# Optimization experiments

Measured on AMD Instinct MI355X. Metric: run time of the kernel, lower is better.

Reference implementation:

```python
import jax, jax.numpy as jnp
import numpy as np

# config (matches SS2Dv2 defaults: d_model=96, d_state=16, ssm_ratio=2.0, dt_rank=auto=6, k_group=4)
DM, DI, N, K, R = 96, 192, 16, 4, 6
BSZ, H_, W_ = 1, 56, 56


def setup_inputs() -> dict:
    key = jax.random.key(0)
    ks = jax.random.split(key, 8)
    return {
        "x": jax.random.normal(ks[0], (BSZ, H_, W_, DM), jnp.float32),
        "in_proj_w": jax.random.normal(ks[1], (2 * DI, DM), jnp.float32) / np.sqrt(DM).astype(np.float32),
        "conv_w": jax.random.normal(ks[2], (DI, 1, 3, 3), jnp.float32) * 0.1,
        "conv_b": jnp.zeros((DI,), jnp.float32),
        "x_proj_w": jax.random.normal(ks[3], (K, R + 2 * N, DI), jnp.float32) / np.sqrt(DI).astype(np.float32),
        "dt_projs_w": 0.1 * jax.random.uniform(ks[4], (K, DI, R), jnp.float32),
        "dt_projs_bias": 0.1 * jax.random.uniform(ks[5], (K, DI), jnp.float32),
        "A_logs": jnp.zeros((K * DI, N), jnp.float32),
        "Ds": jnp.ones((K * DI,), jnp.float32),
        "ln_w": jnp.ones((DI,), jnp.float32),
        "ln_b": jnp.zeros((DI,), jnp.float32),
        "out_proj_w": jax.random.normal(ks[6], (DM, DI), jnp.float32) / np.sqrt(DI).astype(np.float32),
    }


def _cross_scan(x):
    # x: (B, D, H, W) -> (B, 4, D, L); dirs: row-major, col-major, and their flips
    B, D, H, W = x.shape
    L = H * W
    x0 = x.reshape(B, D, L)
    x1 = jnp.swapaxes(x, 2, 3).reshape(B, D, L)
    return jnp.stack([x0, x1, x0[..., ::-1], x1[..., ::-1]], axis=1)


def _cross_merge(ys, H, W):
    # ys: (B, K, D, L) -> (B, D, L); invert each scan direction and sum
    B, Kk, D, L = ys.shape
    y0 = ys[:, 0]
    y2 = ys[:, 2][..., ::-1]
    y1 = jnp.swapaxes(ys[:, 1].reshape(B, D, W, H), 2, 3).reshape(B, D, L)
    y3 = jnp.swapaxes(ys[:, 3][..., ::-1].reshape(B, D, W, H), 2, 3).reshape(B, D, L)
    return y0 + y1 + y2 + y3


def _forward(x, in_proj_w, conv_w, conv_b, x_proj_w, dt_projs_w, dt_projs_bias,
             A_logs, Ds, ln_w, ln_b, out_proj_w):
    B, H, W, _ = x.shape
    L = H * W
    # in_proj + gate split (channel_first=False -> last dim)
    xz = jnp.einsum('bhwc,oc->bhwo', x, in_proj_w)
    xc, z = jnp.split(xz, 2, axis=-1)
    z = jax.nn.silu(z)
    # depthwise conv (NCHW)
    xc = jnp.transpose(xc, (0, 3, 1, 2))
    xc = jax.lax.conv_general_dilated(
        xc, conv_w, (1, 1), 'SAME', feature_group_count=DI,
        dimension_numbers=('NCHW', 'OIHW', 'NCHW')) + conv_b[None, :, None, None]
    xc = jax.nn.silu(xc)
    # 4-directional cross scan
    xs = _cross_scan(xc)  # (B,K,D,L)
    # grouped x_proj: per direction D -> R+2N
    x_dbl = jnp.einsum('bkdl,krd->bkrl', xs, x_proj_w)
    dts, Bs, Cs = jnp.split(x_dbl, [R, R + N], axis=2)  # (B,K,R,L),(B,K,N,L),(B,K,N,L)
    # grouped dt proj: per direction R -> D
    dts = jnp.einsum('bkrl,kdr->bkdl', dts, dt_projs_w)
    A = -jnp.exp(A_logs.astype(jnp.float32)).reshape(K, DI, N)
    delta = jax.nn.softplus(dts + dt_projs_bias[None, :, :, None])  # (B,K,D,L)
    # S6 selective scan: h_t = exp(delta*A)*h_{t-1} + delta*B*u, y_t = C.h_t + D*u
    dA = jnp.exp(jnp.einsum('bkdl,kdn->bkdln', delta, A))
    dBu = jnp.einsum('bkdl,bknl,bkdl->bkdln', delta, Bs, xs)

    def comb(e1, e2):
        a1, b1 = e1
        a2, b2 = e2
        return a2 * a1, a2 * b1 + b2

    _, h = jax.lax.associative_scan(comb, (dA, dBu), axis=3)  # (B,K,D,L,N)
    y = jnp.einsum('bkdln,bknl->bkdl', h, Cs) + Ds.reshape(K, DI)[None, :, :, None] * xs
    y = _cross_merge(y, H, W).reshape(B, DI, H, W)
    # out_norm: LayerNorm over channels (channel_first=False path)
    y = jnp.transpose(y, (0, 2, 3, 1))  # (B,H,W,D)
    mu = y.mean(-1, keepdims=True)
    var = ((y - mu) ** 2).mean(-1, keepdims=True)
    y = (y - mu) / jnp.sqrt(var + 1e-5) * ln_w + ln_b
    y = y * z
    return jnp.einsum('bhwd,od->bhwo', y, out_proj_w)


def reference(x, in_proj_w, conv_w, conv_b, x_proj_w, dt_projs_w, dt_projs_bias,
              A_logs, Ds, ln_w, ln_b, out_proj_w):
    return _forward(x, in_proj_w, conv_w, conv_b, x_proj_w, dt_projs_w, dt_projs_bias,
                    A_logs, Ds, ln_w, ln_b, out_proj_w)
```

## Files before the change

### kernel.cpp

```cpp
#include <hip/hip_runtime.h>
#include <hip/hip_bf16.h>
#include <math.h>

#define DM 96
#define DI 192
#define NS 16
#define KK 4
#define RR 6
#define HH 56
#define WW 56
#define LL (HH*WW)
#define RN (RR + 2*NS)
#define NCH 64
#define CLL (LL/NCH)

__device__ __forceinline__ float silu_f(float x) { return x / (1.f + __expf(-x)); }
__device__ __forceinline__ float softplus_f(float x) {
    return (x > 20.f) ? x : log1pf(__expf(x));
}

__global__ __launch_bounds__(256) void k_inproj(
        const float* __restrict__ x, const float* __restrict__ w,
        float* __restrict__ xc_t, float* __restrict__ z_nat) {
    __shared__ float xt[32 * 100];
    __shared__ float wt[32 * 100];
    const int l0 = blockIdx.x * 32;
    const int o0 = blockIdx.y * 32;
    const int tid = threadIdx.x;
    for (int i = tid; i < 32 * 24; i += 256) {
        int r = i / 24, q = i % 24;
        *(float4*)&xt[r * 100 + 4 * q] = *(const float4*)&x[(size_t)(l0 + r) * DM + 4 * q];
        *(float4*)&wt[r * 100 + 4 * q] = *(const float4*)&w[(size_t)(o0 + r) * DM + 4 * q];
    }
    __syncthreads();
    const int tx = tid & 15, ty = tid >> 4;
    float acc[2][2] = {};
    for (int c = 0; c < 96; c += 4) {
        float4 av[2], bv[2];
#pragma unroll
        for (int i = 0; i < 2; ++i) av[i] = *(const float4*)&xt[(ty + 16 * i) * 100 + c];
#pragma unroll
        for (int j = 0; j < 2; ++j) bv[j] = *(const float4*)&wt[(tx + 16 * j) * 100 + c];
#pragma unroll
        for (int i = 0; i < 2; ++i)
#pragma unroll
            for (int j = 0; j < 2; ++j) {
                acc[i][j] = fmaf(av[i].x, bv[j].x, acc[i][j]);
                acc[i][j] = fmaf(av[i].y, bv[j].y, acc[i][j]);
                acc[i][j] = fmaf(av[i].z, bv[j].z, acc[i][j]);
                acc[i][j] = fmaf(av[i].w, bv[j].w, acc[i][j]);
            }
    }
    __syncthreads();
    float* ot = xt;
#pragma unroll
    for (int j = 0; j < 2; ++j)
#pragma unroll
        for (int i = 0; i < 2; ++i)
            ot[(tx + 16 * j) * 65 + (ty + 16 * i)] = acc[i][j];
    __syncthreads();
    if (o0 < DI) {
        for (int i = tid; i < 32 * 32; i += 256) {
            int ol = i >> 5, ll = i & 31;
            xc_t[(size_t)(o0 + ol) * LL + l0 + ll] = ot[ol * 65 + ll];
        }
    } else {
        for (int i = tid; i < 32 * 32; i += 256) {
            int ll = i >> 5, ol = i & 31;
            z_nat[(size_t)(l0 + ll) * DI + (o0 - DI) + ol] = silu_f(ot[ol * 65 + ll]);
        }
    }
}

__global__ __launch_bounds__(256) void k_convT(
        const float* __restrict__ xc_t, const float* __restrict__ cw,
        const float* __restrict__ cb, float* __restrict__ xconv, float* __restrict__ xs1) {
    __shared__ float in_s[16 * 56];
    __shared__ float out_s[14 * 57];
    const int d = blockIdx.x;
    const int h0 = blockIdx.y * 14;
    const int tid = threadIdx.x;
    const float* in = xc_t + (size_t)d * LL;
    for (int i = tid; i < 16 * 14; i += 256) {
        int row = i / 14, q = i % 14;
        int r = row - 1 + h0;
        float4 v = make_float4(0.f, 0.f, 0.f, 0.f);
        if (r >= 0 && r < HH) v = *(const float4*)&in[r * WW + 4 * q];
        *(float4*)&in_s[row * 56 + 4 * q] = v;
    }
    __syncthreads();
    const float b0 = cb[d];
    float w9[9];
#pragma unroll
    for (int i = 0; i < 9; ++i) w9[i] = cw[d * 9 + i];
    for (int i = tid; i < 14 * 56; i += 256) {
        int hh = i / 56, w = i % 56;
        float acc = b0;
#pragma unroll
        for (int di = 0; di < 3; ++di)
#pragma unroll
            for (int dj = 0; dj < 3; ++dj) {
                int w2 = w + dj - 1;
                if (w2 < 0 || w2 >= WW) continue;
                acc = fmaf(in_s[(hh + di) * 56 + w2], w9[di * 3 + dj], acc);
            }
        acc = silu_f(acc);
        xconv[(size_t)d * LL + (h0 + hh) * WW + w] = acc;
        out_s[hh * 57 + w] = acc;
    }
    __syncthreads();
    for (int i = tid; i < 14 * 56; i += 256) {
        int w = i / 14, hh = i % 14;
        xs1[(size_t)d * LL + w * HH + h0 + hh] = out_s[hh * 57 + w];
    }
}

__global__ __launch_bounds__(256) void k_xdblD(
        const float* __restrict__ xconv, const float* __restrict__ xs1,
        const float* __restrict__ pw, const float* __restrict__ dtw,
        const float* __restrict__ dtb,
        float* __restrict__ Bn, float* __restrict__ Cn, float* __restrict__ delta) {
    __shared__ float xt[DI * 16];
    __shared__ float wk_s[32 * DI];
    __shared__ float dtS[RR * 17];
    const int k = blockIdx.y;
    const int l0 = blockIdx.x * 16;
    const int tid = threadIdx.x;
    const float* in = (k & 1) ? xs1 : xconv;
    const float* wk = pw + (size_t)k * RN * DI;
    for (int i = tid; i < DI * 4; i += 256) {
        int d = i >> 2, q = i & 3;
        *(float4*)&xt[(d << 4) + 4 * q] = *(const float4*)&in[(size_t)d * LL + l0 + 4 * q];
    }
    {
        const float4* src = (const float4*)(wk + RR * DI);
        float4* dst = (float4*)wk_s;
        for (int i = tid; i < (32 * DI) / 4; i += 256) dst[i] = src[i];
    }
    __syncthreads();
    if (tid < RR * 16) {
        int r = tid >> 4, lx = tid & 15;
        const float* wr = wk + r * DI;
        float acc = 0.f;
#pragma unroll 8
        for (int d = 0; d < DI; ++d) acc = fmaf(xt[(d << 4) + lx], wr[d], acc);
        dtS[r * 17 + lx] = acc;
    }
    {
        const int sx = tid & 15, cg = tid >> 4;
        float acc2[2] = {};
        for (int d = 0; d < DI; d += 4) {
            float x0 = xt[(d + 0) * 16 + sx];
            float x1 = xt[(d + 1) * 16 + sx];
            float x2 = xt[(d + 2) * 16 + sx];
            float x3 = xt[(d + 3) * 16 + sx];
#pragma unroll
            for (int j = 0; j < 2; ++j) {
                float4 wv = *(const float4*)&wk_s[(cg + 16 * j) * DI + d];
                acc2[j] = fmaf(x0, wv.x, acc2[j]);
                acc2[j] = fmaf(x1, wv.y, acc2[j]);
                acc2[j] = fmaf(x2, wv.z, acc2[j]);
                acc2[j] = fmaf(x3, wv.w, acc2[j]);
            }
        }
        int s = l0 + sx;
        int ss = (k < 2) ? s : (LL - 1 - s);
        int cch = ss / CLL, ttl = ss - cch * CLL;
        size_t idx = ((size_t)k * LL + (size_t)ttl * NCH + cch) * NS + cg;
        Bn[idx] = acc2[0];
        Cn[idx] = acc2[1];
    }
    __syncthreads();
    for (int oi = tid; oi < DI * 16; oi += 256) {
        int d = oi >> 4, sl = oi & 15;
        int kd = k * DI + d;
        const float* wr = dtw + (size_t)kd * RR;
        float acc = dtb[kd];
#pragma unroll
        for (int r = 0; r < RR; ++r) acc = fmaf(dtS[r * 17 + sl], wr[r], acc);
        delta[(size_t)kd * LL + l0 + sl] = softplus_f(acc);
    }
}

template<int STP, bool TRANS>
__device__ __forceinline__ void scan_dir2(
        const float* sD0, const float* sU0,
        const float* sD1, const float* sU1,
        const float* __restrict__ pB, const float* __restrict__ pC,
        float4 An0, float4 An1, float Dv0, float Dv1, int c, int n,
        float* __restrict__ sP, float* __restrict__ sH,
        float* __restrict__ yg0, float* __restrict__ yg1,
        float* ys0, float* ys1,
        int im0) {
    float sd0 = 0.f, sd1 = 0.f;
    float4 h0 = make_float4(0.f, 0.f, 0.f, 0.f);
    float4 h1 = make_float4(0.f, 0.f, 0.f, 0.f);
#pragma unroll 7
    for (int tl = 0; tl < CLL; ++tl) {
        float dl0 = sD0[STP * tl], u0 = sU0[STP * tl];
        float dl1 = sD1[STP * tl], u1 = sU1[STP * tl];
        float4 Bv = *(const float4*)&pB[(size_t)tl * (NCH * NS)];
        float du0 = dl0 * u0, du1 = dl1 * u1;
        h0.x = fmaf(__builtin_amdgcn_exp2f(dl0 * An0.x), h0.x, du0 * Bv.x);
        h0.y = fmaf(__builtin_amdgcn_exp2f(dl0 * An0.y), h0.y, du0 * Bv.y);
        h0.z = fmaf(__builtin_amdgcn_exp2f(dl0 * An0.z), h0.z, du0 * Bv.z);
        h0.w = fmaf(__builtin_amdgcn_exp2f(dl0 * An0.w), h0.w, du0 * Bv.w);
        h1.x = fmaf(__builtin_amdgcn_exp2f(dl1 * An1.x), h1.x, du1 * Bv.x);
        h1.y = fmaf(__builtin_amdgcn_exp2f(dl1 * An1.y), h1.y, du1 * Bv.y);
        h1.z = fmaf(__builtin_amdgcn_exp2f(dl1 * An1.z), h1.z, du1 * Bv.z);
        h1.w = fmaf(__builtin_amdgcn_exp2f(dl1 * An1.w), h1.w, du1 * Bv.w);
        sd0 += dl0; sd1 += dl1;
    }
    *(float4*)&sP[c * NS + 4 * n] = make_float4(
        __builtin_amdgcn_exp2f(sd0 * An0.x), __builtin_amdgcn_exp2f(sd0 * An0.y),
        __builtin_amdgcn_exp2f(sd0 * An0.z), __builtin_amdgcn_exp2f(sd0 * An0.w));
    *(float4*)&sH[c * NS + 4 * n] = h0;
    __syncthreads();
    float4 hin0 = make_float4(0.f, 0.f, 0.f, 0.f);
    for (int cc = 0; cc < c; ++cc) {
        float4 P  = *(const float4*)&sP[cc * NS + 4 * n];
        float4 Hh = *(const float4*)&sH[cc * NS + 4 * n];
        hin0.x = fmaf(P.x, hin0.x, Hh.x);
        hin0.y = fmaf(P.y, hin0.y, Hh.y);
        hin0.z = fmaf(P.z, hin0.z, Hh.z);
        hin0.w = fmaf(P.w, hin0.w, Hh.w);
    }
    __syncthreads();
    *(float4*)&sP[c * NS + 4 * n] = make_float4(
        __builtin_amdgcn_exp2f(sd1 * An1.x), __builtin_amdgcn_exp2f(sd1 * An1.y),
        __builtin_amdgcn_exp2f(sd1 * An1.z), __builtin_amdgcn_exp2f(sd1 * An1.w));
    *(float4*)&sH[c * NS + 4 * n] = h1;
    __syncthreads();
    float4 hin1 = make_float4(0.f, 0.f, 0.f, 0.f);
    for (int cc = 0; cc < c; ++cc) {
        float4 P  = *(const float4*)&sP[cc * NS + 4 * n];
        float4 Hh = *(const float4*)&sH[cc * NS + 4 * n];
        hin1.x = fmaf(P.x, hin1.x, Hh.x);
        hin1.y = fmaf(P.y, hin1.y, Hh.y);
        hin1.z = fmaf(P.z, hin1.z, Hh.z);
        hin1.w = fmaf(P.w, hin1.w, Hh.w);
    }

    float4 h20 = hin0, h21 = hin1;
    float yr0[13], yr1[13];
#pragma unroll 7
    for (int tl = 0; tl < CLL; ++tl) {
        float dl0 = sD0[STP * tl], u0 = sU0[STP * tl];
        float dl1 = sD1[STP * tl], u1 = sU1[STP * tl];
        float4 Bv = *(const float4*)&pB[(size_t)tl * (NCH * NS)];
        float4 Cv = *(const float4*)&pC[(size_t)tl * (NCH * NS)];
        float du0 = dl0 * u0, du1 = dl1 * u1;
        h20.x = fmaf(__builtin_amdgcn_exp2f(dl0 * An0.x), h20.x, du0 * Bv.x);
        h20.y = fmaf(__builtin_amdgcn_exp2f(dl0 * An0.y), h20.y, du0 * Bv.y);
        h20.z = fmaf(__builtin_amdgcn_exp2f(dl0 * An0.z), h20.z, du0 * Bv.z);
        h20.w = fmaf(__builtin_amdgcn_exp2f(dl0 * An0.w), h20.w, du0 * Bv.w);
        h21.x = fmaf(__builtin_amdgcn_exp2f(dl1 * An1.x), h21.x, du1 * Bv.x);
        h21.y = fmaf(__builtin_amdgcn_exp2f(dl1 * An1.y), h21.y, du1 * Bv.y);
        h21.z = fmaf(__builtin_amdgcn_exp2f(dl1 * An1.z), h21.z, du1 * Bv.z);
        h21.w = fmaf(__builtin_amdgcn_exp2f(dl1 * An1.w), h21.w, du1 * Bv.w);
        float a0 = h20.x * Cv.x;
        a0 = fmaf(h20.y, Cv.y, a0);
        a0 = fmaf(h20.z, Cv.z, a0);
        a0 = fmaf(h20.w, Cv.w, a0);
        float a1 = h21.x * Cv.x;
        a1 = fmaf(h21.y, Cv.y, a1);
        a1 = fmaf(h21.z, Cv.z, a1);
        a1 = fmaf(h21.w, Cv.w, a1);
        a0 += __shfl_xor(a0, 2, 64);
        a0 += __shfl_xor(a0, 1, 64);
        a1 += __shfl_xor(a1, 2, 64);
        a1 += __shfl_xor(a1, 1, 64);
        a0 = fmaf(Dv0, u0, a0);
        a1 = fmaf(Dv1, u1, a1);
        if ((tl & 3) == n) { yr0[tl >> 2] = a0; yr1[tl >> 2] = a1; }
    }
    if (!TRANS) {
#pragma unroll
        for (int j = 0; j < 12; ++j) {
            yg0[STP * (j * 4 + n)] = yr0[j];
            yg1[STP * (j * 4 + n)] = yr1[j];
        }
        if (n == 0) {
            yg0[STP * 48] = yr0[12];
            yg1[STP * 48] = yr1[12];
        }
    } else {
        __syncthreads();
#pragma unroll
        for (int j = 0; j < 12; ++j) {
            int im = im0 + STP * (j * 4 + n);
            int w = im / HH, hh = im - w * HH;
            ys0[hh * 57 + w] = yr0[j];
            ys1[hh * 57 + w] = yr1[j];
        }
        if (n == 0) {
            int im = im0 + STP * 48;
            int w = im / HH, hh = im - w * HH;
            ys0[hh * 57 + w] = yr0[12];
            ys1[hh * 57 + w] = yr1[12];
        }
    }
}

__global__ __launch_bounds__(256) void k_scan(
        const float* __restrict__ delta, const float* __restrict__ Bn,
        const float* __restrict__ Cn,
        const float* __restrict__ xconv, const float* __restrict__ xs1,
        const float* __restrict__ A_logs, const float* __restrict__ Ds,
        float* __restrict__ y4) {
    __shared__ float sbuf[4 * LL];
    __shared__ float sP[NCH * NS];
    __shared__ float sH[NCH * NS];
    int b = blockIdx.x;
    int k = b / (DI / 2), dp = b % (DI / 2);
    int d0 = 2 * dp;
    int tid = threadIdx.x;
    int c = tid >> 2, n = tid & 3;
    int kd0 = k * DI + d0;
    const float LOG2E = 1.4426950408889634f;
    float4 Alg0 = *(const float4*)&A_logs[(size_t)kd0 * NS + 4 * n];
    float4 Alg1 = *(const float4*)&A_logs[(size_t)(kd0 + 1) * NS + 4 * n];
    float4 An0 = make_float4(-__expf(Alg0.x) * LOG2E, -__expf(Alg0.y) * LOG2E,
                             -__expf(Alg0.z) * LOG2E, -__expf(Alg0.w) * LOG2E);
    float4 An1 = make_float4(-__expf(Alg1.x) * LOG2E, -__expf(Alg1.y) * LOG2E,
                             -__expf(Alg1.z) * LOG2E, -__expf(Alg1.w) * LOG2E);
    float Dv0 = Ds[kd0], Dv1 = Ds[kd0 + 1];
    const float* del0 = delta + (size_t)kd0 * LL;
    const float* uP0  = ((k & 1) ? xs1 : xconv) + (size_t)d0 * LL;
    {
        const float4* s1 = (const float4*)del0;
        const float4* s2 = (const float4*)uP0;
        float4* dst = (float4*)sbuf;
        for (int i = tid; i < LL / 2; i += 256) {
            dst[i] = s1[i];
            dst[LL / 2 + i] = s2[i];
        }
    }
    __syncthreads();
    const float* Bb = Bn + (size_t)k * LL * NS + c * NS + 4 * n;
    const float* Cb = Cn + (size_t)k * LL * NS + c * NS + 4 * n;
    float* yo0 = y4 + (size_t)kd0 * LL;
    float* yo1 = yo0 + LL;
    float* ys0 = sbuf;
    float* ys1 = sbuf + 57 * 56;
    const int t0 = c * CLL;
    const int imF = t0;
    const int imR = LL - 1 - t0;
    const float* sD0 = sbuf;
    const float* sD1 = sbuf + LL;
    const float* sU0 = sbuf + 2 * LL;
    const float* sU1 = sbuf + 3 * LL;
    if (k == 0) {
        scan_dir2<1, false>(sD0 + imF, sU0 + imF, sD1 + imF, sU1 + imF, Bb, Cb,
                            An0, An1, Dv0, Dv1, c, n, sP, sH,
                            yo0 + imF, yo1 + imF, nullptr, nullptr, 0);
    } else if (k == 1) {
        scan_dir2<1, true>(sD0 + imF, sU0 + imF, sD1 + imF, sU1 + imF, Bb, Cb,
                           An0, An1, Dv0, Dv1, c, n, sP, sH,
                           nullptr, nullptr, ys0, ys1, imF);
    } else if (k == 2) {
        scan_dir2<-1, false>(sD0 + imR, sU0 + imR, sD1 + imR, sU1 + imR, Bb, Cb,
                             An0, An1, Dv0, Dv1, c, n, sP, sH,
                             yo0 + imR, yo1 + imR, nullptr, nullptr, 0);
    } else {
        scan_dir2<-1, true>(sD0 + imR, sU0 + imR, sD1 + imR, sU1 + imR, Bb, Cb,
                            An0, An1, Dv0, Dv1, c, n, sP, sH,
                            nullptr, nullptr, ys0, ys1, imR);
    }
    if (k & 1) {
        __syncthreads();
        for (int p = tid; p < LL; p += 256) {
            yo0[p] = ys0[p + p / WW];
            yo1[p] = ys1[p + p / WW];
        }
    }
}

__global__ __launch_bounds__(256) void k_lnout(
        const float* __restrict__ y4, const float* __restrict__ z_nat,
        const float* __restrict__ lnw, const float* __restrict__ lnb,
        const float* __restrict__ ow, float* __restrict__ out) {
    __shared__ float yv[16 * 196];
    __shared__ float ow_s[48 * 196];
    __shared__ float mean_s[16], inv_s[16];
    const int l0 = blockIdx.x * 16;
    const int pass = blockIdx.y;
    const int tid = threadIdx.x;
    for (int i = tid; i < 48 * 48; i += 256) {
        int o = i / 48, q = i % 48;
        *(float4*)&ow_s[o * 196 + 4 * q] =
            *(const float4*)&ow[(size_t)(pass * 48 + o) * DI + 4 * q];
    }
    for (int i = tid; i < DI * 4; i += 256) {
        int d = i >> 2, q = i & 3;
        size_t off = (size_t)d * LL + l0 + 4 * q;
        float4 a = *(const float4*)&y4[off];
        float4 b = *(const float4*)&y4[(size_t)DI * LL + off];
        float4 c2 = *(const float4*)&y4[(size_t)(2 * DI) * LL + off];
        float4 e = *(const float4*)&y4[(size_t)(3 * DI) * LL + off];
        int p = 4 * q;
        yv[(p + 0) * 196 + d] = a.x + b.x + c2.x + e.x;
        yv[(p + 1) * 196 + d] = a.y + b.y + c2.y + e.y;
        yv[(p + 2) * 196 + d] = a.z + b.z + c2.z + e.z;
        yv[(p + 3) * 196 + d] = a.w + b.w + c2.w + e.w;
    }
    __syncthreads();
    {
        int p = tid >> 4, e = tid & 15;
        float s1 = 0.f;
#pragma unroll
        for (int m = 0; m < 12; ++m) s1 += yv[p * 196 + e + 16 * m];
        s1 += __shfl_xor(s1, 8, 64);
        s1 += __shfl_xor(s1, 4, 64);
        s1 += __shfl_xor(s1, 2, 64);
        s1 += __shfl_xor(s1, 1, 64);
        float mean = s1 * (1.f / DI);
        float s2 = 0.f;
#pragma unroll
        for (int m = 0; m < 12; ++m) {
            float dv = yv[p * 196 + e + 16 * m] - mean;
            s2 = fmaf(dv, dv, s2);
        }
        s2 += __shfl_xor(s2, 8, 64);
        s2 += __shfl_xor(s2, 4, 64);
        s2 += __shfl_xor(s2, 2, 64);
        s2 += __shfl_xor(s2, 1, 64);
        if (e == 0) {
            mean_s[p] = mean;
            inv_s[p] = rsqrtf(s2 * (1.f / DI) + 1e-5f);
        }
    }
    __syncthreads();
    for (int i = tid; i < 16 * 48; i += 256) {
        int p = i / 48, q = i % 48;
        float4 z4 = *(const float4*)&z_nat[(size_t)(l0 + p) * DI + 4 * q];
        float4 w4 = *(const float4*)&lnw[4 * q];
        float4 b4 = *(const float4*)&lnb[4 * q];
        float4 yy = *(const float4*)&yv[p * 196 + 4 * q];
        float m = mean_s[p], iv = inv_s[p];
        yy.x = ((yy.x - m) * iv * w4.x + b4.x) * z4.x;
        yy.y = ((yy.y - m) * iv * w4.y + b4.y) * z4.y;
        yy.z = ((yy.z - m) * iv * w4.z + b4.z) * z4.z;
        yy.w = ((yy.w - m) * iv * w4.w + b4.w) * z4.w;
        *(float4*)&yv[p * 196 + 4 * q] = yy;
    }
    __syncthreads();
    const int ty = tid >> 4, tx = tid & 15;
    float acc[3] = {};
    for (int dd = 0; dd < DI; dd += 4) {
        float4 a0 = *(const float4*)&yv[ty * 196 + dd];
#pragma unroll
        for (int j = 0; j < 3; ++j) {
            float4 bv = *(const float4*)&ow_s[(tx + 16 * j) * 196 + dd];
            acc[j] += a0.x * bv.x + a0.y * bv.y + a0.z * bv.z + a0.w * bv.w;
        }
    }
#pragma unroll
    for (int j = 0; j < 3; ++j)
        out[(size_t)(l0 + ty) * DM + pass * 48 + tx + 16 * j] = acc[j];
}

extern "C" void kernel_launch(void* const* d_in, const int* in_sizes, int n_in,
                              void* d_out, int out_size, void* d_ws, size_t ws_size,
                              hipStream_t stream) {
    const float* x    = (const float*)d_in[0];
    const float* ipw  = (const float*)d_in[1];
    const float* cw   = (const float*)d_in[2];
    const float* cb   = (const float*)d_in[3];
    const float* xpw  = (const float*)d_in[4];
    const float* dtw  = (const float*)d_in[5];
    const float* dtb  = (const float*)d_in[6];
    const float* alog = (const float*)d_in[7];
    const float* Dsp  = (const float*)d_in[8];
    const float* lnw  = (const float*)d_in[9];
    const float* lnb  = (const float*)d_in[10];
    const float* ow   = (const float*)d_in[11];
    float* out = (float*)d_out;

    float* ws     = (float*)d_ws;
    float* xc_t   = ws;
    float* z_nat  = xc_t + DI * LL;
    float* xconv  = z_nat + DI * LL;
    float* xs1    = xconv + DI * LL;
    float* Bn     = xs1 + DI * LL;
    float* Cn     = Bn + (size_t)KK * LL * NS;
    float* delta  = Cn + (size_t)KK * LL * NS;
    float* y4     = delta + (size_t)KK * DI * LL;

    k_inproj <<<dim3(LL / 32, 12), 256, 0, stream>>>(x, ipw, xc_t, z_nat);
    k_convT  <<<dim3(DI, 4), 256, 0, stream>>>(xc_t, cw, cb, xconv, xs1);
    k_xdblD  <<<dim3(LL / 16, KK), 256, 0, stream>>>(xconv, xs1, xpw, dtw, dtb, Bn, Cn, delta);
    k_scan   <<<KK * DI / 2, 256, 0, stream>>>(delta, Bn, Cn, xconv, xs1, alog, Dsp, y4);
    k_lnout  <<<dim3(LL / 16, 2), 256, 0, stream>>>(y4, z_nat, lnw, lnb, ow, out);
}
```

Baseline: 173.8 us.

## Store delta and u chunk-interleaved so scan reads global memory without LDS staging

```diff
diff --git a/kernel.cpp b/kernel.cpp
--- a/kernel.cpp
+++ b/kernel.cpp
@@ -113,6 +113,20 @@
         int w = i / 14, hh = i % 14;
         xs1[(size_t)d * LL + w * HH + h0 + hh] = out_s[hh * 57 + w];
     }
+}
+
+__global__ __launch_bounds__(256) void k_uso(
+        const float* __restrict__ xconv, const float* __restrict__ xs1,
+        float* __restrict__ uA, float* __restrict__ uB) {
+    __shared__ float row[LL];
+    const int d = blockIdx.x;
+    const float* src = (blockIdx.y ? xs1 : xconv) + (size_t)d * LL;
+    float* dst = (blockIdx.y ? uB : uA) + (size_t)d * LL;
+    for (int i = threadIdx.x; i < LL / 4; i += 256)
+        ((float4*)row)[i] = ((const float4*)src)[i];
+    __syncthreads();
+    for (int i = threadIdx.x; i < LL; i += 256)
+        dst[i] = row[(i & (NCH - 1)) * CLL + (i >> 6)];
 }
 
 __global__ __launch_bounds__(256) void k_xdblD(
@@ -178,14 +192,17 @@
         float acc = dtb[kd];
 #pragma unroll
         for (int r = 0; r < RR; ++r) acc = fmaf(dtS[r * 17 + sl], wr[r], acc);
-        delta[(size_t)kd * LL + l0 + sl] = softplus_f(acc);
+        int s = l0 + sl;
+        int ss = (k < 2) ? s : (LL - 1 - s);
+        int cch = ss / CLL, ttl = ss - cch * CLL;
+        delta[(size_t)kd * LL + (size_t)ttl * NCH + cch] = softplus_f(acc);
     }
 }
 
 template<int STP, bool TRANS>
 __device__ __forceinline__ void scan_dir2(
-        const float* sD0, const float* sU0,
-        const float* sD1, const float* sU1,
+        const float* __restrict__ pd0, const float* __restrict__ pd1,
+        const float* __restrict__ pu0, const float* __restrict__ pu1,
         const float* __restrict__ pB, const float* __restrict__ pC,
         float4 An0, float4 An1, float Dv0, float Dv1, int c, int n,
         float* __restrict__ sP, float* __restrict__ sH,
@@ -197,8 +214,8 @@
     float4 h1 = make_float4(0.f, 0.f, 0.f, 0.f);
 #pragma unroll 7
     for (int tl = 0; tl < CLL; ++tl) {
-        float dl0 = sD0[STP * tl], u0 = sU0[STP * tl];
-        float dl1 = sD1[STP * tl], u1 = sU1[STP * tl];
+        float dl0 = pd0[tl * NCH], dl1 = pd1[tl * NCH];
+        float u0 = pu0[STP * NCH * tl], u1 = pu1[STP * NCH * tl];
         float4 Bv = *(const float4*)&pB[(size_t)tl * (NCH * NS)];
         float du0 = dl0 * u0, du1 = dl1 * u1;
         h0.x = fmaf(__builtin_amdgcn_exp2f(dl0 * An0.x), h0.x, du0 * Bv.x);
@@ -242,11 +259,10 @@
     }
 
     float4 h20 = hin0, h21 = hin1;
-    float yr0[13], yr1[13];
 #pragma unroll 7
     for (int tl = 0; tl < CLL; ++tl) {
-        float dl0 = sD0[STP * tl], u0 = sU0[STP * tl];
-        float dl1 = sD1[STP * tl], u1 = sU1[STP * tl];
+        float dl0 = pd0[tl * NCH], dl1 = pd1[tl * NCH];
+        float u0 = pu0[STP * NCH * tl], u1 = pu1[STP * NCH * tl];
         float4 Bv = *(const float4*)&pB[(size_t)tl * (NCH * NS)];
         float4 Cv = *(const float4*)&pC[(size_t)tl * (NCH * NS)];
         float du0 = dl0 * u0, du1 = dl1 * u1;
@@ -272,32 +288,16 @@
         a1 += __shfl_xor(a1, 1, 64);
         a0 = fmaf(Dv0, u0, a0);
         a1 = fmaf(Dv1, u1, a1);
-        if ((tl & 3) == n) { yr0[tl >> 2] = a0; yr1[tl >> 2] = a1; }
-    }
-    if (!TRANS) {
-#pragma unroll
-        for (int j = 0; j < 12; ++j) {
-            yg0[STP * (j * 4 + n)] = yr0[j];
-            yg1[STP * (j * 4 + n)] = yr1[j];
-        }
-        if (n == 0) {
-            yg0[STP * 48] = yr0[12];
-            yg1[STP * 48] = yr1[12];
-        }
-    } else {
-        __syncthreads();
-#pragma unroll
-        for (int j = 0; j < 12; ++j) {
-            int im = im0 + STP * (j * 4 + n);
-            int w = im / HH, hh = im - w * HH;
-            ys0[hh * 57 + w] = yr0[j];
-            ys1[hh * 57 + w] = yr1[j];
-        }
-        if (n == 0) {
-            int im = im0 + STP * 48;
-            int w = im / HH, hh = im - w * HH;
-            ys0[hh * 57 + w] = yr0[12];
-            ys1[hh * 57 + w] = yr1[12];
+        if ((tl & 3) == n) {
+            if (!TRANS) {
+                yg0[STP * tl] = a0;
+                yg1[STP * tl] = a1;
+            } else {
+                int im = im0 + STP * tl;
+                int w = im / HH, hh = im - w * HH;
+                ys0[hh * 57 + w] = a0;
+                ys1[hh * 57 + w] = a1;
+            }
         }
     }
 }
@@ -305,12 +305,13 @@
 __global__ __launch_bounds__(256) void k_scan(
         const float* __restrict__ delta, const float* __restrict__ Bn,
         const float* __restrict__ Cn,
-        const float* __restrict__ xconv, const float* __restrict__ xs1,
+        const float* __restrict__ uA, const float* __restrict__ uB,
         const float* __restrict__ A_logs, const float* __restrict__ Ds,
         float* __restrict__ y4) {
-    __shared__ float sbuf[4 * LL];
     __shared__ float sP[NCH * NS];
     __shared__ float sH[NCH * NS];
+    __shared__ float ys0[HH * 57];
+    __shared__ float ys1[HH * 57];
     int b = blockIdx.x;
     int k = b / (DI / 2), dp = b % (DI / 2);
     int d0 = 2 * dp;
@@ -325,45 +326,31 @@
     float4 An1 = make_float4(-__expf(Alg1.x) * LOG2E, -__expf(Alg1.y) * LOG2E,
                              -__expf(Alg1.z) * LOG2E, -__expf(Alg1.w) * LOG2E);
     float Dv0 = Ds[kd0], Dv1 = Ds[kd0 + 1];
-    const float* del0 = delta + (size_t)kd0 * LL;
-    const float* uP0  = ((k & 1) ? xs1 : xconv) + (size_t)d0 * LL;
-    {
-        const float4* s1 = (const float4*)del0;
-        const float4* s2 = (const float4*)uP0;
-        float4* dst = (float4*)sbuf;
-        for (int i = tid; i < LL / 2; i += 256) {
-            dst[i] = s1[i];
-            dst[LL / 2 + i] = s2[i];
-        }
-    }
-    __syncthreads();
+    const float* pd0 = delta + (size_t)kd0 * LL + c;
+    const float* pd1 = pd0 + LL;
+    const float* ub0 = ((k & 1) ? uB : uA) + (size_t)d0 * LL;
+    const float* ub1 = ub0 + LL;
     const float* Bb = Bn + (size_t)k * LL * NS + c * NS + 4 * n;
     const float* Cb = Cn + (size_t)k * LL * NS + c * NS + 4 * n;
     float* yo0 = y4 + (size_t)kd0 * LL;
     float* yo1 = yo0 + LL;
-    float* ys0 = sbuf;
-    float* ys1 = sbuf + 57 * 56;
     const int t0 = c * CLL;
     const int imF = t0;
     const int imR = LL - 1 - t0;
-    const float* sD0 = sbuf;
-    const float* sD1 = sbuf + LL;
-    const float* sU0 = sbuf + 2 * LL;
-    const float* sU1 = sbuf + 3 * LL;
     if (k == 0) {
-        scan_dir2<1, false>(sD0 + imF, sU0 + imF, sD1 + imF, sU1 + imF, Bb, Cb,
+        scan_dir2<1, false>(pd0, pd1, ub0 + c, ub1 + c, Bb, Cb,
                             An0, An1, Dv0, Dv1, c, n, sP, sH,
                             yo0 + imF, yo1 + imF, nullptr, nullptr, 0);
     } else if (k == 1) {
-        scan_dir2<1, true>(sD0 + imF, sU0 + imF, sD1 + imF, sU1 + imF, Bb, Cb,
+        scan_dir2<1, true>(pd0, pd1, ub0 + c, ub1 + c, Bb, Cb,
                            An0, An1, Dv0, Dv1, c, n, sP, sH,
                            nullptr, nullptr, ys0, ys1, imF);
     } else if (k == 2) {
-        scan_dir2<-1, false>(sD0 + imR, sU0 + imR, sD1 + imR, sU1 + imR, Bb, Cb,
+        scan_dir2<-1, false>(pd0, pd1, ub0 + (LL - 1) - c, ub1 + (LL - 1) - c, Bb, Cb,
                              An0, An1, Dv0, Dv1, c, n, sP, sH,
                              yo0 + imR, yo1 + imR, nullptr, nullptr, 0);
     } else {
-        scan_dir2<-1, true>(sD0 + imR, sU0 + imR, sD1 + imR, sU1 + imR, Bb, Cb,
+        scan_dir2<-1, true>(pd0, pd1, ub0 + (LL - 1) - c, ub1 + (LL - 1) - c, Bb, Cb,
                             An0, An1, Dv0, Dv1, c, n, sP, sH,
                             nullptr, nullptr, ys0, ys1, imR);
     }
@@ -482,14 +469,17 @@
     float* z_nat  = xc_t + DI * LL;
     float* xconv  = z_nat + DI * LL;
     float* xs1    = xconv + DI * LL;
-    float* Bn     = xs1 + DI * LL;
+    float* uA     = xs1 + DI * LL;
+    float* uB     = uA + DI * LL;
+    float* Bn     = uB + DI * LL;
     float* Cn     = Bn + (size_t)KK * LL * NS;
     float* delta  = Cn + (size_t)KK * LL * NS;
     float* y4     = delta + (size_t)KK * DI * LL;
 
     k_inproj <<<dim3(LL / 32, 12), 256, 0, stream>>>(x, ipw, xc_t, z_nat);
     k_convT  <<<dim3(DI, 4), 256, 0, stream>>>(xc_t, cw, cb, xconv, xs1);
+    k_uso    <<<dim3(DI, 2), 256, 0, stream>>>(xconv, xs1, uA, uB);
     k_xdblD  <<<dim3(LL / 16, KK), 256, 0, stream>>>(xconv, xs1, xpw, dtw, dtb, Bn, Cn, delta);
-    k_scan   <<<KK * DI / 2, 256, 0, stream>>>(delta, Bn, Cn, xconv, xs1, alog, Dsp, y4);
+    k_scan   <<<KK * DI / 2, 256, 0, stream>>>(delta, Bn, Cn, uA, uB, alog, Dsp, y4);
     k_lnout  <<<dim3(LL / 16, 2), 256, 0, stream>>>(y4, z_nat, lnw, lnb, ow, out);
 }
```

New measurement: 202.5 us. 1.17x slower.
